# Performance work log

Measured on AMD Instinct MI355X. Metric: run time of the kernel, lower is better.

## Reference

```python
import jax, jax.numpy as jnp
import numpy as np

IN_DIM, HIDDEN_DIM, LATENT_DIM = 512, 1024, 256
B, N = 64, 1024


def setup_inputs() -> dict:
    key = jax.random.key(0)
    ks = jax.random.split(key, 8)
    x = jax.random.normal(ks[0], (B, N, IN_DIM), dtype=jnp.float32)
    a = jax.random.uniform(ks[1], (B, N, N), dtype=jnp.float32)
    s1 = 1.0 / np.sqrt(IN_DIM)
    s2 = 1.0 / np.sqrt(HIDDEN_DIM)
    W1 = jax.random.uniform(ks[2], (HIDDEN_DIM, IN_DIM), jnp.float32, -s1, s1)
    b1 = jax.random.uniform(ks[3], (HIDDEN_DIM,), jnp.float32, -s1, s1)
    W_mu = jax.random.uniform(ks[4], (LATENT_DIM, HIDDEN_DIM), jnp.float32, -s2, s2)
    b_mu = jax.random.uniform(ks[5], (LATENT_DIM,), jnp.float32, -s2, s2)
    W_lv = jax.random.uniform(ks[6], (LATENT_DIM, HIDDEN_DIM), jnp.float32, -s2, s2)
    b_lv = jax.random.uniform(ks[7], (LATENT_DIM,), jnp.float32, -s2, s2)
    return {"x": x, "a": a, "W1": W1, "b1": b1, "W_mu": W_mu, "b_mu": b_mu,
            "W_lv": W_lv, "b_lv": b_lv}


def normalize_adj(a):
    # A_hat = A + I; D^{-1/2} A_hat D^{-1/2} expressed as row/col scaling
    n = a.shape[-1]
    a_hat = a + jnp.eye(n, dtype=a.dtype)
    deg = a_hat.sum(axis=-1)                      # [B, N]
    d = (deg + 1e-8) ** -0.5                      # [B, N]
    return a_hat * d[..., :, None] * d[..., None, :]


def reference(x, a, W1, b1, W_mu, b_mu, W_lv, b_lv):
    a_norm = normalize_adj(a)                     # [B, N, N]
    h = jnp.einsum('bnm,bmd->bnd', a_norm, x)     # message passing
    h = jax.nn.relu(jnp.einsum('bnd,hd->bnh', h, W1) + b1)
    mu = jnp.einsum('bnh,lh->bnl', h, W_mu) + b_mu
    logvar = jnp.einsum('bnh,lh->bnl', h, W_lv) + b_lv
    return (mu, logvar)
```

## Files before the change

### kernel.cpp

```cpp
#include <hip/hip_runtime.h>
#include <hip/hip_bf16.h>
#include <type_traits>

typedef unsigned short u16;
typedef __attribute__((ext_vector_type(8))) short s16x8;
typedef __attribute__((ext_vector_type(4))) float f32x4;

__device__ __forceinline__ u16 f2bf(float f) {
    union { float f; unsigned u; } c; c.f = f;
    unsigned r = c.u + 0x7fffu + ((c.u >> 16) & 1u);
    return (u16)(r >> 16);
}

template<bool CVT>
__global__ __launch_bounds__(256) void rowsum_kernel(const float* __restrict__ a,
                                                     float* __restrict__ dsc,
                                                     u16* __restrict__ ab) {
    const int wave = threadIdx.x >> 6, lane = threadIdx.x & 63;
    const long row = (long)blockIdx.x * 4 + wave;
    const float4* a4 = (const float4*)(a + row * 1024);
    float s = 0.f;
    #pragma unroll
    for (int i = 0; i < 4; ++i) {
        float4 v = a4[i * 64 + lane];
        if (CVT) {
            union { u16 u[4]; uint2 w; } cv;
            cv.u[0] = f2bf(v.x); cv.u[1] = f2bf(v.y);
            cv.u[2] = f2bf(v.z); cv.u[3] = f2bf(v.w);
            *(uint2*)(ab + row * 1024 + (long)(i * 64 + lane) * 4) = cv.w;
        }
        s += v.x + v.y + v.z + v.w;
    }
    #pragma unroll
    for (int off = 32; off > 0; off >>= 1) s += __shfl_down(s, off, 64);
    if (lane == 0) dsc[row] = rsqrtf(s + 1.0f + 1e-8f);
}

__global__ __launch_bounds__(256) void xst_kernel(const float* __restrict__ x,
                                                  const float* __restrict__ dsc,
                                                  u16* __restrict__ xst) {
    __shared__ u16 ls[64][65];
    const int b  = blockIdx.z;
    const int n0 = blockIdx.x * 64;
    const int j0 = blockIdx.y * 64;
    const int t  = threadIdx.x;
    {
        int jj = t >> 4, nn = (t & 15) * 4;
        #pragma unroll
        for (int it = 0; it < 4; ++it, jj += 16) {
            float dj = dsc[b * 1024 + j0 + jj];
            float4 v = *(const float4*)(x + ((long)(b * 1024 + j0 + jj)) * 512 + n0 + nn);
            ls[jj][nn + 0] = f2bf(v.x * dj);
            ls[jj][nn + 1] = f2bf(v.y * dj);
            ls[jj][nn + 2] = f2bf(v.z * dj);
            ls[jj][nn + 3] = f2bf(v.w * dj);
        }
    }
    __syncthreads();
    {
        int nn = t >> 2;
        int jv = (t & 3) * 8;
        #pragma unroll
        for (int it = 0; it < 2; ++it, jv += 32) {
            union { u16 u[8]; uint4 w; } cv;
            #pragma unroll
            for (int u = 0; u < 8; ++u) cv.u[u] = ls[jv + u][nn];
            *(uint4*)(xst + ((long)b * 512 + n0 + nn) * 1024 + j0 + jv) = cv.w;
        }
    }
}

__global__ __launch_bounds__(256) void cvt_weights(const float* __restrict__ W1,
                                                   const float* __restrict__ Wmu,
                                                   const float* __restrict__ Wlv,
                                                   u16* __restrict__ w1b,
                                                   u16* __restrict__ wml) {
    int i = blockIdx.x * 256 + threadIdx.x;
    w1b[i] = f2bf(W1[i]);
    wml[i] = f2bf(i < 262144 ? Wmu[i] : Wlv[i - 262144]);
}

template<int EPI, typename TA>
__global__ __launch_bounds__(256) void gemm_bt(
    const TA* __restrict__ A, const u16* __restrict__ Bt,
    int K, long aBStride, long bBStride,
    const float* __restrict__ dsc, const float* __restrict__ xin,
    u16* __restrict__ outb,
    const float* __restrict__ bias0, const float* __restrict__ bias1,
    float* __restrict__ outMu, float* __restrict__ outLv)
{
    __shared__ __align__(16) u16 As[128 * 40];
    __shared__ __align__(16) u16 Bs[128 * 40];
    const int bz = blockIdx.z;
    const TA* Ab = A + (long)bz * aBStride;
    const u16* Bb = Bt + (long)bz * bBStride;
    const int n0 = blockIdx.x * 128, m0 = blockIdx.y * 128;
    const int t = threadIdx.x;
    const int wave = t >> 6, lane = t & 63, quad = lane >> 4, tr = lane & 15;
    const int wm = (wave >> 1) * 64, wn = (wave & 1) * 64;

    f32x4 acc[4][4];
    #pragma unroll
    for (int i = 0; i < 4; ++i)
        #pragma unroll
        for (int j = 0; j < 4; ++j) acc[i][j] = (f32x4){0.f, 0.f, 0.f, 0.f};

    const int mm = t >> 2, kk = (t & 3) * 8;
    for (int k0 = 0; k0 < K; k0 += 32) {
        #pragma unroll
        for (int it = 0; it < 2; ++it) {
            const int r = mm + it * 64;
            if constexpr (std::is_same<TA, float>::value) {
                const float4* p = (const float4*)(Ab + (long)(m0 + r) * K + k0 + kk);
                float4 v0 = p[0], v1 = p[1];
                union { u16 u[8]; uint4 w; } cv;
                cv.u[0]=f2bf(v0.x); cv.u[1]=f2bf(v0.y); cv.u[2]=f2bf(v0.z); cv.u[3]=f2bf(v0.w);
                cv.u[4]=f2bf(v1.x); cv.u[5]=f2bf(v1.y); cv.u[6]=f2bf(v1.z); cv.u[7]=f2bf(v1.w);
                *(uint4*)&As[r * 40 + kk] = cv.w;
            } else {
                uint4 v = *(const uint4*)(Ab + (long)(m0 + r) * K + k0 + kk);
                *(uint4*)&As[r * 40 + kk] = v;
            }
        }
        #pragma unroll
        for (int it = 0; it < 2; ++it) {
            const int r = mm + it * 64;
            uint4 v = *(const uint4*)(Bb + (long)(n0 + r) * K + k0 + kk);
            *(uint4*)&Bs[r * 40 + kk] = v;
        }
        __syncthreads();
        s16x8 af[4], bfv[4];
        #pragma unroll
        for (int mi = 0; mi < 4; ++mi)
            af[mi] = *(const s16x8*)&As[(wm + mi * 16 + tr) * 40 + quad * 8];
        #pragma unroll
        for (int ni = 0; ni < 4; ++ni)
            bfv[ni] = *(const s16x8*)&Bs[(wn + ni * 16 + tr) * 40 + quad * 8];
        #pragma unroll
        for (int mi = 0; mi < 4; ++mi)
            #pragma unroll
            for (int ni = 0; ni < 4; ++ni)
                acc[mi][ni] = __builtin_amdgcn_mfma_f32_16x16x32_bf16(af[mi], bfv[ni], acc[mi][ni], 0, 0, 0);
        __syncthreads();
    }

    #pragma unroll
    for (int mi = 0; mi < 4; ++mi) {
        #pragma unroll
        for (int ni = 0; ni < 4; ++ni) {
            const int gn = n0 + wn + ni * 16 + tr;
            #pragma unroll
            for (int r = 0; r < 4; ++r) {
                const int gm = m0 + wm + mi * 16 + quad * 4 + r;
                float v = acc[mi][ni][r];
                if constexpr (EPI == 1) {
                    long row = (long)bz * 1024 + gm;
                    float di = dsc[row];
                    float xv = xin[row * 512 + gn];
                    outb[row * 512 + gn] = f2bf(di * (v + di * xv));
                } else if constexpr (EPI == 2) {
                    float hv = v + bias0[gn];
                    outb[(long)gm * 1024 + gn] = f2bf(hv > 0.f ? hv : 0.f);
                } else {
                    if (gn < 256) outMu[(long)gm * 256 + gn] = v + bias0[gn];
                    else          outLv[(long)gm * 256 + (gn - 256)] = v + bias1[gn - 256];
                }
            }
        }
    }
}

extern "C" void kernel_launch(void* const* d_in, const int* in_sizes, int n_in,
                              void* d_out, int out_size, void* d_ws, size_t ws_size,
                              hipStream_t stream) {
    const float* x   = (const float*)d_in[0];
    const float* a   = (const float*)d_in[1];
    const float* W1  = (const float*)d_in[2];
    const float* b1  = (const float*)d_in[3];
    const float* Wmu = (const float*)d_in[4];
    const float* bmu = (const float*)d_in[5];
    const float* Wlv = (const float*)d_in[6];
    const float* blv = (const float*)d_in[7];
    float* out = (float*)d_out;

    char* base = (char*)d_ws;
    size_t off = 0;
    auto take = [&](size_t bytes) { char* p = base + off; off += (bytes + 255) & ~(size_t)255; return p; };
    float* dsc = (float*)take((size_t)65536 * 4);
    u16*  xst  = (u16*)take((size_t)64 * 512 * 1024 * 2);
    u16*  h    = (u16*)take((size_t)65536 * 512 * 2);
    u16*  hid  = (u16*)take((size_t)65536 * 1024 * 2);
    u16*  w1b  = (u16*)take((size_t)1024 * 512 * 2);
    u16*  wml  = (u16*)take((size_t)512 * 1024 * 2);
    u16*  ab   = (u16*)take((size_t)64 * 1024 * 1024 * 2);
    const bool useAb = (off <= ws_size);

    if (useAb) rowsum_kernel<true ><<<16384, 256, 0, stream>>>(a, dsc, ab);
    else       rowsum_kernel<false><<<16384, 256, 0, stream>>>(a, dsc, nullptr);
    xst_kernel<<<dim3(8, 16, 64), 256, 0, stream>>>(x, dsc, xst);
    cvt_weights<<<2048, 256, 0, stream>>>(W1, Wmu, Wlv, w1b, wml);

    if (useAb)
        gemm_bt<1, u16><<<dim3(4, 8, 64), 256, 0, stream>>>(
            ab, xst, 1024, 1024L * 1024, 512L * 1024,
            dsc, x, h, nullptr, nullptr, nullptr, nullptr);
    else
        gemm_bt<1, float><<<dim3(4, 8, 64), 256, 0, stream>>>(
            a, xst, 1024, 1024L * 1024, 512L * 1024,
            dsc, x, h, nullptr, nullptr, nullptr, nullptr);

    gemm_bt<2, u16><<<dim3(8, 512, 1), 256, 0, stream>>>(
        h, w1b, 512, 0, 0, nullptr, nullptr, hid, b1, nullptr, nullptr, nullptr);

    gemm_bt<3, u16><<<dim3(4, 512, 1), 256, 0, stream>>>(
        hid, wml, 1024, 0, 0, nullptr, nullptr, nullptr, bmu, blv,
        out, out + (size_t)65536 * 256);
}
```

Measured before the change: 929.4 us.

## Load GEMM tiles directly into LDS and fold identity into bf16 adjacency

The bf16-operand GEMMs now stage tiles with global_load_lds, which writes global memory straight into LDS without a register round trip. The LDS row pitch drops from 40 to 32 elements, so bank conflicts on fragment reads may rise. The rowsum kernel also adds the +1 diagonal into the bf16 adjacency copy, so the first GEMM epilogue no longer reads x in fp32. That makes the diagonal term pass through bf16 rounding. A separate fp32-A kernel keeps the old path for when the workspace is too small.

Result: faster. 875.9 us (-5.8%).

```diff
diff --git a/kernel.cpp b/kernel.cpp
--- a/kernel.cpp
+++ b/kernel.cpp
@@ -10,6 +10,12 @@
     union { float f; unsigned u; } c; c.f = f;
     unsigned r = c.u + 0x7fffu + ((c.u >> 16) & 1u);
     return (u16)(r >> 16);
+}
+
+__device__ __forceinline__ void gld_lds16(const u16* g, u16* l) {
+    __builtin_amdgcn_global_load_lds(
+        (const __attribute__((address_space(1))) void*)g,
+        (__attribute__((address_space(3))) void*)l, 16, 0, 0);
 }
 
 template<bool CVT>
@@ -18,18 +24,22 @@
                                                      u16* __restrict__ ab) {
     const int wave = threadIdx.x >> 6, lane = threadIdx.x & 63;
     const long row = (long)blockIdx.x * 4 + wave;
+    const int diag = (int)(row & 1023);
     const float4* a4 = (const float4*)(a + row * 1024);
     float s = 0.f;
     #pragma unroll
     for (int i = 0; i < 4; ++i) {
         float4 v = a4[i * 64 + lane];
+        s += v.x + v.y + v.z + v.w;
         if (CVT) {
+            const int c0 = (i * 64 + lane) * 4;
+            float e[4] = {v.x, v.y, v.z, v.w};
+            if (diag >= c0 && diag < c0 + 4) e[diag - c0] += 1.0f;
             union { u16 u[4]; uint2 w; } cv;
-            cv.u[0] = f2bf(v.x); cv.u[1] = f2bf(v.y);
-            cv.u[2] = f2bf(v.z); cv.u[3] = f2bf(v.w);
-            *(uint2*)(ab + row * 1024 + (long)(i * 64 + lane) * 4) = cv.w;
-        }
-        s += v.x + v.y + v.z + v.w;
+            cv.u[0] = f2bf(e[0]); cv.u[1] = f2bf(e[1]);
+            cv.u[2] = f2bf(e[2]); cv.u[3] = f2bf(e[3]);
+            *(uint2*)(ab + row * 1024 + c0) = cv.w;
+        }
     }
     #pragma unroll
     for (int off = 32; off > 0; off >>= 1) s += __shfl_down(s, off, 64);
@@ -80,62 +90,50 @@
     wml[i] = f2bf(i < 262144 ? Wmu[i] : Wlv[i - 262144]);
 }
 
-template<int EPI, typename TA>
-__global__ __launch_bounds__(256) void gemm_bt(
-    const TA* __restrict__ A, const u16* __restrict__ Bt,
+template<int EPI>
+__global__ __launch_bounds__(256) void gemm_lds(
+    const u16* __restrict__ A, const u16* __restrict__ Bt,
     int K, long aBStride, long bBStride,
-    const float* __restrict__ dsc, const float* __restrict__ xin,
+    const float* __restrict__ dsc,
     u16* __restrict__ outb,
     const float* __restrict__ bias0, const float* __restrict__ bias1,
     float* __restrict__ outMu, float* __restrict__ outLv)
 {
-    __shared__ __align__(16) u16 As[128 * 40];
-    __shared__ __align__(16) u16 Bs[128 * 40];
+    __shared__ __align__(16) u16 As[128 * 32];
+    __shared__ __align__(16) u16 Bs[128 * 32];
     const int bz = blockIdx.z;
-    const TA* Ab = A + (long)bz * aBStride;
+    const u16* Ab = A + (long)bz * aBStride;
     const u16* Bb = Bt + (long)bz * bBStride;
     const int n0 = blockIdx.x * 128, m0 = blockIdx.y * 128;
     const int t = threadIdx.x;
     const int wave = t >> 6, lane = t & 63, quad = lane >> 4, tr = lane & 15;
     const int wm = (wave >> 1) * 64, wn = (wave & 1) * 64;
 
+    const int srowA = wave * 32 + (lane >> 2);
+    const int scol  = (lane & 3) * 8;
+    u16* ldsA0 = As + wave * 1024;
+    u16* ldsB0 = Bs + wave * 1024;
+
     f32x4 acc[4][4];
     #pragma unroll
     for (int i = 0; i < 4; ++i)
         #pragma unroll
         for (int j = 0; j < 4; ++j) acc[i][j] = (f32x4){0.f, 0.f, 0.f, 0.f};
 
-    const int mm = t >> 2, kk = (t & 3) * 8;
     for (int k0 = 0; k0 < K; k0 += 32) {
         #pragma unroll
         for (int it = 0; it < 2; ++it) {
-            const int r = mm + it * 64;
-            if constexpr (std::is_same<TA, float>::value) {
-                const float4* p = (const float4*)(Ab + (long)(m0 + r) * K + k0 + kk);
-                float4 v0 = p[0], v1 = p[1];
-                union { u16 u[8]; uint4 w; } cv;
-                cv.u[0]=f2bf(v0.x); cv.u[1]=f2bf(v0.y); cv.u[2]=f2bf(v0.z); cv.u[3]=f2bf(v0.w);
-                cv.u[4]=f2bf(v1.x); cv.u[5]=f2bf(v1.y); cv.u[6]=f2bf(v1.z); cv.u[7]=f2bf(v1.w);
-                *(uint4*)&As[r * 40 + kk] = cv.w;
-            } else {
-                uint4 v = *(const uint4*)(Ab + (long)(m0 + r) * K + k0 + kk);
-                *(uint4*)&As[r * 40 + kk] = v;
-            }
-        }
-        #pragma unroll
-        for (int it = 0; it < 2; ++it) {
-            const int r = mm + it * 64;
-            uint4 v = *(const uint4*)(Bb + (long)(n0 + r) * K + k0 + kk);
-            *(uint4*)&Bs[r * 40 + kk] = v;
+            gld_lds16(Ab + (long)(m0 + srowA + it * 16) * K + k0 + scol, ldsA0 + it * 512);
+            gld_lds16(Bb + (long)(n0 + srowA + it * 16) * K + k0 + scol, ldsB0 + it * 512);
         }
         __syncthreads();
         s16x8 af[4], bfv[4];
         #pragma unroll
         for (int mi = 0; mi < 4; ++mi)
-            af[mi] = *(const s16x8*)&As[(wm + mi * 16 + tr) * 40 + quad * 8];
+            af[mi] = *(const s16x8*)&As[(wm + mi * 16 + tr) * 32 + quad * 8];
         #pragma unroll
         for (int ni = 0; ni < 4; ++ni)
-            bfv[ni] = *(const s16x8*)&Bs[(wn + ni * 16 + tr) * 40 + quad * 8];
+            bfv[ni] = *(const s16x8*)&Bs[(wn + ni * 16 + tr) * 32 + quad * 8];
         #pragma unroll
         for (int mi = 0; mi < 4; ++mi)
             #pragma unroll
@@ -155,9 +153,7 @@
                 float v = acc[mi][ni][r];
                 if constexpr (EPI == 1) {
                     long row = (long)bz * 1024 + gm;
-                    float di = dsc[row];
-                    float xv = xin[row * 512 + gn];
-                    outb[row * 512 + gn] = f2bf(di * (v + di * xv));
+                    outb[row * 512 + gn] = f2bf(dsc[row] * v);
                 } else if constexpr (EPI == 2) {
                     float hv = v + bias0[gn];
                     outb[(long)gm * 1024 + gn] = f2bf(hv > 0.f ? hv : 0.f);
@@ -168,6 +164,72 @@
             }
         }
     }
+}
+
+__global__ __launch_bounds__(256) void gemm_f32a(
+    const float* __restrict__ A, const u16* __restrict__ Bt,
+    const float* __restrict__ dsc, const float* __restrict__ xin,
+    u16* __restrict__ outb)
+{
+    __shared__ __align__(16) u16 As[128 * 40];
+    __shared__ __align__(16) u16 Bs[128 * 40];
+    const int bz = blockIdx.z;
+    const float* Ab = A + (long)bz * 1024 * 1024;
+    const u16* Bb = Bt + (long)bz * 512 * 1024;
+    const int n0 = blockIdx.x * 128, m0 = blockIdx.y * 128;
+    const int t = threadIdx.x;
+    const int wave = t >> 6, lane = t & 63, quad = lane >> 4, tr = lane & 15;
+    const int wm = (wave >> 1) * 64, wn = (wave & 1) * 64;
+    const int K = 1024;
+
+    f32x4 acc[4][4];
+    #pragma unroll
+    for (int i = 0; i < 4; ++i)
+        #pragma unroll
+        for (int j = 0; j < 4; ++j) acc[i][j] = (f32x4){0.f, 0.f, 0.f, 0.f};
+
+    const int mm = t >> 2, kk = (t & 3) * 8;
+    for (int k0 = 0; k0 < K; k0 += 32) {
+        #pragma unroll
+        for (int it = 0; it < 2; ++it) {
+            const int r = mm + it * 64;
+            const float4* p = (const float4*)(Ab + (long)(m0 + r) * K + k0 + kk);
+            float4 v0 = p[0], v1 = p[1];
+            union { u16 u[8]; uint4 w; } cv;
+            cv.u[0]=f2bf(v0.x); cv.u[1]=f2bf(v0.y); cv.u[2]=f2bf(v0.z); cv.u[3]=f2bf(v0.w);
+            cv.u[4]=f2bf(v1.x); cv.u[5]=f2bf(v1.y); cv.u[6]=f2bf(v1.z); cv.u[7]=f2bf(v1.w);
+            *(uint4*)&As[r * 40 + kk] = cv.w;
+            uint4 v = *(const uint4*)(Bb + (long)(n0 + r) * K + k0 + kk);
+            *(uint4*)&Bs[r * 40 + kk] = v;
+        }
+        __syncthreads();
+        s16x8 af[4], bfv[4];
+        #pragma unroll
+        for (int mi = 0; mi < 4; ++mi)
+            af[mi] = *(const s16x8*)&As[(wm + mi * 16 + tr) * 40 + quad * 8];
+        #pragma unroll
+        for (int ni = 0; ni < 4; ++ni)
+            bfv[ni] = *(const s16x8*)&Bs[(wn + ni * 16 + tr) * 40 + quad * 8];
+        #pragma unroll
+        for (int mi = 0; mi < 4; ++mi)
+            #pragma unroll
+            for (int ni = 0; ni < 4; ++ni)
+                acc[mi][ni] = __builtin_amdgcn_mfma_f32_16x16x32_bf16(af[mi], bfv[ni], acc[mi][ni], 0, 0, 0);
+        __syncthreads();
+    }
+    #pragma unroll
+    for (int mi = 0; mi < 4; ++mi)
+        #pragma unroll
+        for (int ni = 0; ni < 4; ++ni) {
+            const int gn = n0 + wn + ni * 16 + tr;
+            #pragma unroll
+            for (int r = 0; r < 4; ++r) {
+                const int gm = m0 + wm + mi * 16 + quad * 4 + r;
+                long row = (long)bz * 1024 + gm;
+                float di = dsc[row];
+                outb[row * 512 + gn] = f2bf(di * (acc[mi][ni][r] + di * xin[row * 512 + gn]));
+            }
+        }
 }
 
 extern "C" void kernel_launch(void* const* d_in, const int* in_sizes, int n_in,
@@ -201,18 +263,16 @@
     cvt_weights<<<2048, 256, 0, stream>>>(W1, Wmu, Wlv, w1b, wml);
 
     if (useAb)
-        gemm_bt<1, u16><<<dim3(4, 8, 64), 256, 0, stream>>>(
+        gemm_lds<1><<<dim3(4, 8, 64), 256, 0, stream>>>(
             ab, xst, 1024, 1024L * 1024, 512L * 1024,
-            dsc, x, h, nullptr, nullptr, nullptr, nullptr);
+            dsc, h, nullptr, nullptr, nullptr, nullptr);
     else
-        gemm_bt<1, float><<<dim3(4, 8, 64), 256, 0, stream>>>(
-            a, xst, 1024, 1024L * 1024, 512L * 1024,
-            dsc, x, h, nullptr, nullptr, nullptr, nullptr);
-
-    gemm_bt<2, u16><<<dim3(8, 512, 1), 256, 0, stream>>>(
-        h, w1b, 512, 0, 0, nullptr, nullptr, hid, b1, nullptr, nullptr, nullptr);
-
-    gemm_bt<3, u16><<<dim3(4, 512, 1), 256, 0, stream>>>(
-        hid, wml, 1024, 0, 0, nullptr, nullptr, nullptr, bmu, blv,
+        gemm_f32a<<<dim3(4, 8, 64), 256, 0, stream>>>(a, xst, dsc, x, h);
+
+    gemm_lds<2><<<dim3(8, 512, 1), 256, 0, stream>>>(
+        h, w1b, 512, 0, 0, nullptr, hid, b1, nullptr, nullptr, nullptr);
+
+    gemm_lds<3><<<dim3(4, 512, 1), 256, 0, stream>>>(
+        hid, wml, 1024, 0, 0, nullptr, nullptr, bmu, blv,
         out, out + (size_t)65536 * 256);
 }
```
